# Kernel tuning notes

Measured on AMD Instinct MI355X. Metric: run time of the kernel, lower is better.

Reference implementation:

```python
import jax, jax.numpy as jnp
import numpy as np

NUM_HEADS = 12


def get_rel_pos(q_size, k_size, rel_pos):
    # relative coordinate lookup (q_size == k_size here; table has 2*size >= 2*size-1 rows)
    idx = jnp.arange(q_size)[:, None] - jnp.arange(k_size)[None, :] + (k_size - 1)
    return rel_pos[idx]  # [q_size, k_size, head_dim]


def setup_inputs() -> dict:
    key = jax.random.key(0)
    ks = jax.random.split(key, 5)
    B, H, W, E = 8, 32, 32, 768
    hd = E // NUM_HEADS
    x = jax.random.normal(ks[0], (B, H, W, E), jnp.float32)
    Wqkv = jax.random.normal(ks[1], (E, 3 * E), jnp.float32) * (E ** -0.5)
    bqkv = jnp.zeros((3 * E,), jnp.float32)
    Wproj = jax.random.normal(ks[2], (E, E), jnp.float32) * (E ** -0.5)
    bproj = jnp.zeros((E,), jnp.float32)
    rel_pos_h = jax.random.normal(ks[3], (2 * H, hd), jnp.float32) * 0.02
    rel_pos_w = jax.random.normal(ks[4], (2 * W, hd), jnp.float32) * 0.02
    return dict(x=x, Wqkv=Wqkv, bqkv=bqkv, Wproj=Wproj, bproj=bproj,
                rel_pos_h=rel_pos_h, rel_pos_w=rel_pos_w)


def reference(x, Wqkv, bqkv, Wproj, bproj, rel_pos_h, rel_pos_w):
    B, H, W, E = x.shape
    nh = NUM_HEADS
    hd = E // nh
    N = H * W
    scale = hd ** -0.5
    # QKV projection, then the exact reshape/transpose sequence of the TF module
    qkv = x.reshape(B, N, E) @ Wqkv + bqkv                       # [B, N, 3E]
    qkv = qkv.reshape(B, N, nh, hd, 3).transpose(0, 1, 2, 4, 3)  # [B, N, nh, 3, hd]
    qkv = qkv.reshape(B * nh, N, hd, 3)                          # raw row-major reshape (faithful)
    q, k, v = qkv[..., 0], qkv[..., 1], qkv[..., 2]              # each [B*nh, N, hd]
    attn = jnp.einsum('bnd,bmd->bnm', q * scale, k)              # [B*nh, N, N]
    # decomposed relative position bias (SAM-style)
    Rh = get_rel_pos(H, H, rel_pos_h)                            # [H, H, hd]
    Rw = get_rel_pos(W, W, rel_pos_w)                            # [W, W, hd]
    r_q = q.reshape(B * nh, H, W, hd)
    rel_h = jnp.einsum('bhwc,hkc->bhwk', r_q, Rh)                # [B*nh, H, W, H]
    rel_w = jnp.einsum('bhwc,wkc->bhwk', r_q, Rw)                # [B*nh, H, W, W]
    attn = (attn.reshape(B * nh, H, W, H, W)
            + rel_h[..., :, None]
            + rel_w[..., None, :]).reshape(B * nh, N, N)
    attn = jax.nn.softmax(attn, axis=-1)
    out = attn @ v                                               # [B*nh, N, hd]
    # faithful raw reshape + transpose back to [B, H, W, E]
    out = out.reshape(B, H, W, nh, hd).transpose(0, 3, 1, 2, 4).reshape(B, H, W, nh * hd)
    return out @ Wproj + bproj
```

## Files before the change

### kernel.cpp

```cpp
#include <hip/hip_runtime.h>
#include <hip/hip_bf16.h>


typedef __attribute__((ext_vector_type(8))) short short8;
typedef __attribute__((ext_vector_type(4))) float f32x4;

__global__ __launch_bounds__(256) void cast_f32_bf16(const float* __restrict__ in,
                                                     __hip_bfloat16* __restrict__ out) {
  int i = (blockIdx.x * 256 + threadIdx.x) * 4;
  float4 v = *(const float4*)&in[i];
  out[i + 0] = __float2bfloat16(v.x);
  out[i + 1] = __float2bfloat16(v.y);
  out[i + 2] = __float2bfloat16(v.z);
  out[i + 3] = __float2bfloat16(v.w);
}

__global__ __launch_bounds__(256) void transpose_cast(const float* __restrict__ in,
                                                      __hip_bfloat16* __restrict__ out,
                                                      int K, int N) {
  __shared__ float tile[32][33];
  int n0 = blockIdx.x * 32, k0 = blockIdx.y * 32;
  int tx = threadIdx.x & 31, ty = threadIdx.x >> 5;
#pragma unroll
  for (int i = 0; i < 4; ++i)
    tile[ty + i * 8][tx] = in[(size_t)(k0 + ty + i * 8) * N + n0 + tx];
  __syncthreads();
#pragma unroll
  for (int i = 0; i < 4; ++i)
    out[(size_t)(n0 + ty + i * 8) * K + k0 + tx] = __float2bfloat16(tile[tx][ty + i * 8]);
}

__device__ inline void gload16(const void* g, void* l) {
  __builtin_amdgcn_global_load_lds((const __attribute__((address_space(1))) void*)g,
                                   (__attribute__((address_space(3))) void*)l, 16, 0, 0);
}

template<int BM, bool OUT_BF16>
__global__ __launch_bounds__(256) void gemm_pipe(const __hip_bfloat16* __restrict__ A,
                                                 const __hip_bfloat16* __restrict__ Bt,
                                                 const float* __restrict__ bias,
                                                 void* __restrict__ Cout,
                                                 int N, int K) {
  constexpr int FM = BM / 32;
  constexpr int ABYTES = BM * 128;
  constexpr int AOPW = BM / 32;
  __shared__ __align__(16) char lds[2 * ABYTES + 2 * 16384];
  char* Abuf = lds;
  char* Bbuf = lds + 2 * ABYTES;
  int n0 = blockIdx.x * 128, m0 = blockIdx.y * BM;
  int tid = threadIdx.x, lane = tid & 63, wid = tid >> 6;
  int wm = wid >> 1, wn = wid & 1;
  int lr = lane & 15, lg = lane >> 4;
  int xr = lr & 7;
  int g_ = lane >> 3;
  int colsw = ((lane & 7) ^ g_) * 8;
  f32x4 acc[FM][4] = {};

#pragma unroll
  for (int j = 0; j < AOPW; ++j) {
    int op = wid * AOPW + j;
    gload16(&A[(size_t)(m0 + op * 8 + g_) * K + colsw], Abuf + op * 1024);
  }
#pragma unroll
  for (int j = 0; j < 4; ++j) {
    int op = wid * 4 + j;
    gload16(&Bt[(size_t)(n0 + op * 8 + g_) * K + colsw], Bbuf + op * 1024);
  }

  int cur = 0;
#pragma unroll 1
  for (int k0 = 0; k0 < K; k0 += 64) {
    __builtin_amdgcn_sched_barrier(0);
    __builtin_amdgcn_s_barrier();
    int kn = (k0 + 64 < K) ? k0 + 64 : k0;
#pragma unroll
    for (int j = 0; j < AOPW; ++j) {
      int op = wid * AOPW + j;
      gload16(&A[(size_t)(m0 + op * 8 + g_) * K + kn + colsw],
              Abuf + (cur ^ 1) * ABYTES + op * 1024);
    }
#pragma unroll
    for (int j = 0; j < 4; ++j) {
      int op = wid * 4 + j;
      gload16(&Bt[(size_t)(n0 + op * 8 + g_) * K + kn + colsw],
              Bbuf + (cur ^ 1) * 16384 + op * 1024);
    }
    if constexpr (BM == 128) asm volatile("s_waitcnt vmcnt(8)" ::: "memory");
    else                     asm volatile("s_waitcnt vmcnt(6)" ::: "memory");
    __builtin_amdgcn_sched_barrier(0);
    __builtin_amdgcn_s_barrier();
    __builtin_amdgcn_sched_barrier(0);

    const char* Ac = Abuf + cur * ABYTES;
    const char* Bc = Bbuf + cur * 16384;
#pragma unroll
    for (int ks = 0; ks < 2; ++ks) {
      short8 af[FM], bfr[4];
#pragma unroll
      for (int m = 0; m < FM; ++m) {
        int row = wm * (BM / 2) + m * 16 + lr;
        af[m] = *(const short8*)(Ac + row * 128 + (((ks * 4 + lg) ^ xr) * 16));
      }
#pragma unroll
      for (int n = 0; n < 4; ++n) {
        int row = wn * 64 + n * 16 + lr;
        bfr[n] = *(const short8*)(Bc + row * 128 + (((ks * 4 + lg) ^ xr) * 16));
      }
#pragma unroll
      for (int m = 0; m < FM; ++m)
#pragma unroll
        for (int n = 0; n < 4; ++n)
          acc[m][n] = __builtin_amdgcn_mfma_f32_16x16x32_bf16(af[m], bfr[n], acc[m][n], 0, 0, 0);
    }
    cur ^= 1;
  }
#pragma unroll
  for (int n = 0; n < 4; ++n) {
    int col = n0 + wn * 64 + n * 16 + lr;
    float bv = bias[col];
#pragma unroll
    for (int m = 0; m < FM; ++m) {
      int rowb = m0 + wm * (BM / 2) + m * 16 + lg * 4;
#pragma unroll
      for (int r = 0; r < 4; ++r) {
        float v = acc[m][n][r] + bv;
        if (OUT_BF16)
          ((__hip_bfloat16*)Cout)[(size_t)(rowb + r) * N + col] = __float2bfloat16(v);
        else
          ((float*)Cout)[(size_t)(rowb + r) * N + col] = v;
      }
    }
  }
}

__global__ __launch_bounds__(256) void permute_v2(const __hip_bfloat16* __restrict__ qkv,
                                                  __hip_bfloat16* __restrict__ Q,
                                                  __hip_bfloat16* __restrict__ Kd,
                                                  __hip_bfloat16* __restrict__ Vt) {
  int bh = blockIdx.y, n0 = blockIdx.x * 64;
  int tid = threadIdx.x;
  __shared__ short raw[64 * 200];
  __shared__ short vt[64][72];
  const short* src = (const short*)qkv + (size_t)(bh * 1024 + n0) * 192;
#pragma unroll
  for (int i = 0; i < 6; ++i) {
    int c16 = tid + i * 256;
    int wi = c16 / 24, off = (c16 % 24) * 8;
    *(short8*)&raw[wi * 200 + off] = *(const short8*)&src[(size_t)c16 * 8];
  }
  __syncthreads();
  int wi = tid >> 2, g4 = tid & 3;
  const short* rw_ = &raw[wi * 200];
  short8 qv[2], kv_[2];
#pragma unroll
  for (int half = 0; half < 2; ++half)
#pragma unroll
    for (int j = 0; j < 8; ++j) {
      int d2 = g4 * 16 + half * 8 + j;
      int u = 3 * d2;
      qv[half][j]  = rw_[((u) & 63) * 3 + ((u) >> 6)];
      kv_[half][j] = rw_[((u + 1) & 63) * 3 + ((u + 1) >> 6)];
      vt[d2][wi]   = rw_[((u + 2) & 63) * 3 + ((u + 2) >> 6)];
    }
  size_t base = (size_t)bh * 65536 + (size_t)(n0 + wi) * 64 + g4 * 16;
  *(short8*)&Q[base] = qv[0];
  *(short8*)&Q[base + 8] = qv[1];
  *(short8*)&Kd[base] = kv_[0];
  *(short8*)&Kd[base + 8] = kv_[1];
  __syncthreads();
  int d2r = tid >> 2;
  size_t vbase = (size_t)bh * 65536 + (size_t)d2r * 1024 + n0 + g4 * 16;
  *(short8*)&Vt[vbase]     = *(const short8*)&vt[d2r][g4 * 16];
  *(short8*)&Vt[vbase + 8] = *(const short8*)&vt[d2r][g4 * 16 + 8];
}

__device__ inline short8 cvt8(const float* p) {
  short8 r;
#pragma unroll
  for (int j = 0; j < 8; ++j) {
    __hip_bfloat16 b = __float2bfloat16(p[j]);
    r[j] = *reinterpret_cast<const short*>(&b);
  }
  return r;
}

__device__ inline unsigned packtrunc(float a, float b) {
  return __builtin_amdgcn_perm(__float_as_uint(b), __float_as_uint(a), 0x07060302u);
}

#define L2E 1.44269504088896f
__global__ __launch_bounds__(512) void attn13(const __hip_bfloat16* __restrict__ Q,
                                              const __hip_bfloat16* __restrict__ Kd,
                                              const __hip_bfloat16* __restrict__ Vt,
                                              const float* __restrict__ rph,
                                              const float* __restrict__ rpw,
                                              __hip_bfloat16* __restrict__ outp) {
  int orig = blockIdx.x;
  int xcd = orig & 7, loc = orig >> 3;
  int bh = xcd * 12 + (loc % 12);
  int qt = loc / 12;
  int tid = threadIdx.x;
  int lane = tid & 63, w = tid >> 6;
  int lr = lane & 15, lg = lane >> 4;
  int xr = lr & 7;

  __shared__ __align__(16) char lds[49152];

  const __hip_bfloat16* Qb = Q + (size_t)bh * 65536;
  const __hip_bfloat16* Kb = Kd + (size_t)bh * 65536;
  const __hip_bfloat16* Vb = Vt + (size_t)bh * 65536;

  int q0 = qt * 128 + w * 16;
  int hq = q0 >> 5;
  int wq_lane = (q0 & 31) + lr;

  short8 qf0 = *(const short8*)&Qb[(size_t)(q0 + lr) * 64 + lg * 8];
  short8 qf1 = *(const short8*)&Qb[(size_t)(q0 + lr) * 64 + 32 + lg * 8];

  char* rhb = lds + 24576 + w * 1024;
#pragma unroll
  for (int kt = 0; kt < 2; ++kt) {
    int row = hq - (kt * 16 + lr) + 31;
    const float* tp = rph + (size_t)row * 64 + lg * 8;
    short8 th0 = cvt8(tp), th1 = cvt8(tp + 32);
    f32x4 a = {};
    a = __builtin_amdgcn_mfma_f32_16x16x32_bf16(qf0, th0, a, 0, 0, 0);
    a = __builtin_amdgcn_mfma_f32_16x16x32_bf16(qf1, th1, a, 0, 0, 0);
#pragma unroll
    for (int r = 0; r < 4; ++r) {
      int q = lg * 4 + r;
      int e = kt * 16 + lr;
      int sw = ((e >> 1) ^ q) << 2;
      *(__hip_bfloat16*)(rhb + q * 64 + sw + (e & 1) * 2) = __float2bfloat16(a[r] * L2E);
    }
  }
  __hip_bfloat16* rwt = (__hip_bfloat16*)(lds + w * 2176);
#pragma unroll
  for (int jt = 0; jt < 4; ++jt) {
    const float* tp = rpw + (size_t)(jt * 16 + lr) * 64 + lg * 8;
    short8 tw0 = cvt8(tp), tw1 = cvt8(tp + 32);
    f32x4 a = {};
    a = __builtin_amdgcn_mfma_f32_16x16x32_bf16(qf0, tw0, a, 0, 0, 0);
    a = __builtin_amdgcn_mfma_f32_16x16x32_bf16(qf1, tw1, a, 0, 0, 0);
#pragma unroll
    for (int r = 0; r < 4; ++r)
      rwt[(lg * 4 + r) * 68 + jt * 16 + lr] = __float2bfloat16(a[r] * L2E);
  }
  float rwreg[8];
#pragma unroll
  for (int i = 0; i < 8; ++i) {
    int k = (i >> 2) * 16 + lg * 4 + (i & 3);
    rwreg[i] = __bfloat162float(rwt[lr * 68 + (wq_lane - k + 31)]);
  }
  __syncthreads();

  f32x4 O[4] = {};
  float m_ = -1e30f, lsum = 0.f;
  const float C = 0.125f * L2E;
  char* pc = lds + 32768 + w * 2048;
  char* vcb = lds + 16384;

  int g_ = lane >> 3;
  int colb = ((lane & 7) ^ g_) * 8;

  gload16(&Kb[(size_t)(w * 8 + g_) * 64 + colb], lds + w * 1024);

  int cur = 0;
#pragma unroll 1
  for (int kv0 = 0; kv0 < 1024; kv0 += 64) {
    __builtin_amdgcn_sched_barrier(0);
    __builtin_amdgcn_s_barrier();
    gload16(&Vb[(size_t)(w * 8 + g_) * 1024 + kv0 + colb], vcb + w * 1024);
    int nkv = (kv0 + 64 < 1024) ? kv0 + 64 : 960;
    gload16(&Kb[(size_t)(nkv + w * 8 + g_) * 64 + colb], lds + (cur ^ 1) * 8192 + w * 1024);
    asm volatile("s_waitcnt vmcnt(2)" ::: "memory");
    __builtin_amdgcn_sched_barrier(0);
    __builtin_amdgcn_s_barrier();
    __builtin_amdgcn_sched_barrier(0);

    const char* kc = lds + cur * 8192;
    short8 kf[8];
#pragma unroll
    for (int t = 0; t < 4; ++t)
#pragma unroll
      for (int h = 0; h < 2; ++h)
        kf[2 * t + h] = *(const short8*)(kc + (t * 16 + lr) * 128 + (((h * 4 + lg) ^ xr) * 16));
    f32x4 st[4];
#pragma unroll
    for (int t = 0; t < 4; ++t) {
      f32x4 z = {};
      z = __builtin_amdgcn_mfma_f32_16x16x32_bf16(kf[2 * t], qf0, z, 0, 0, 0);
      z = __builtin_amdgcn_mfma_f32_16x16x32_bf16(kf[2 * t + 1], qf1, z, 0, 0, 0);
      st[t] = z;
    }
    int s_ = kv0 >> 6;
    unsigned bu = *(const unsigned*)(rhb + lr * 64 + ((s_ ^ lr) << 2));
    float bh0 = __uint_as_float(bu << 16);
    float bh1 = __uint_as_float(bu & 0xffff0000u);
    float mx = -1e30f;
#pragma unroll
    for (int t = 0; t < 4; ++t)
#pragma unroll
      for (int r = 0; r < 4; ++r) {
        float sv = fmaf(st[t][r], C, ((t < 2) ? bh0 : bh1) + rwreg[(t & 1) * 4 + r]);
        st[t][r] = sv;
        mx = fmaxf(mx, sv);
      }
    if (!__all(mx <= m_ + 8.f)) {
      float mw = fmaxf(mx, __shfl_xor(mx, 16, 64));
      mw = fmaxf(mw, __shfl_xor(mw, 32, 64));
      float mnew = fmaxf(m_, mw);
      float al = exp2f(m_ - mnew);
      lsum *= al;
      m_ = mnew;
#pragma unroll
      for (int r = 0; r < 4; ++r) {
        float av = __shfl(al, lg * 4 + r, 64);
#pragma unroll
        for (int dt = 0; dt < 4; ++dt) O[dt][r] *= av;
      }
    }
    float sa = 0.f;
#pragma unroll
    for (int t = 0; t < 4; ++t) {
      float p0 = exp2f(st[t][0] - m_);
      float p1 = exp2f(st[t][1] - m_);
      float p2 = exp2f(st[t][2] - m_);
      float p3 = exp2f(st[t][3] - m_);
      sa += (p0 + p1) + (p2 + p3);
      uint2 wv;
      wv.x = packtrunc(p0, p1);
      wv.y = packtrunc(p2, p3);
      int slot = (2 * t + (lg >> 1)) ^ xr;
      *(uint2*)(pc + lr * 128 + slot * 16 + (lg & 1) * 8) = wv;
    }
    lsum += sa;
    short8 pf0 = *(const short8*)(pc + lr * 128 + (((0 + lg) ^ xr) * 16));
    short8 pf1 = *(const short8*)(pc + lr * 128 + (((4 + lg) ^ xr) * 16));
    asm volatile("s_waitcnt vmcnt(1)" ::: "memory");
    __builtin_amdgcn_sched_barrier(0);
    __builtin_amdgcn_s_barrier();
    __builtin_amdgcn_sched_barrier(0);
#pragma unroll
    for (int dt = 0; dt < 4; ++dt) {
      short8 vf0 = *(const short8*)(vcb + (dt * 16 + lr) * 128 + (((0 + lg) ^ xr) * 16));
      short8 vf1 = *(const short8*)(vcb + (dt * 16 + lr) * 128 + (((4 + lg) ^ xr) * 16));
      O[dt] = __builtin_amdgcn_mfma_f32_16x16x32_bf16(pf0, vf0, O[dt], 0, 0, 0);
      O[dt] = __builtin_amdgcn_mfma_f32_16x16x32_bf16(pf1, vf1, O[dt], 0, 0, 0);
    }
    cur ^= 1;
  }

  float lt = lsum;
  lt += __shfl_xor(lt, 16, 64);
  lt += __shfl_xor(lt, 32, 64);
  float linv = 1.f / lt;
#pragma unroll
  for (int r = 0; r < 4; ++r) {
    float lv = __shfl(linv, lg * 4 + r, 64);
    int n = q0 + lg * 4 + r;
#pragma unroll
    for (int dt = 0; dt < 4; ++dt) {
      int d = dt * 16 + lr;
      int Sidx = bh * 65536 + n * 64 + d;
      int b = Sidx / 786432, r1 = Sidx % 786432;
      int pp = r1 / 24576, r2 = r1 % 24576;
      int qq = r2 / 768, r3 = r2 % 768;
      int j = r3 >> 6, dd = r3 & 63;
      int P = b * 786432 + j * 65536 + pp * 2048 + qq * 64 + dd;
      outp[P] = __float2bfloat16(O[dt][r] * lv);
    }
  }
}

extern "C" void kernel_launch(void* const* d_in, const int* in_sizes, int n_in,
                              void* d_out, int out_size, void* d_ws, size_t ws_size,
                              hipStream_t stream) {
  const float* x     = (const float*)d_in[0];
  const float* Wqkv  = (const float*)d_in[1];
  const float* bqkv  = (const float*)d_in[2];
  const float* Wproj = (const float*)d_in[3];
  const float* bproj = (const float*)d_in[4];
  const float* rph   = (const float*)d_in[5];
  const float* rpw   = (const float*)d_in[6];
  float* out = (float*)d_out;
  char* ws = (char*)d_ws;

  __hip_bfloat16* xb     = (__hip_bfloat16*)(ws);
  __hip_bfloat16* wqkvT  = (__hip_bfloat16*)(ws + 12582912);
  __hip_bfloat16* wprojT = (__hip_bfloat16*)(ws + 16121856);
  __hip_bfloat16* qkvb   = (__hip_bfloat16*)(ws + 17301504);
  __hip_bfloat16* Qm     = (__hip_bfloat16*)(ws + 55050240);
  __hip_bfloat16* Km     = (__hip_bfloat16*)(ws + 67633152);
  __hip_bfloat16* Vtm    = (__hip_bfloat16*)(ws + 80216064);

  cast_f32_bf16<<<dim3(6144), dim3(256), 0, stream>>>(x, xb);
  transpose_cast<<<dim3(72, 24), dim3(256), 0, stream>>>(Wqkv, wqkvT, 768, 2304);
  transpose_cast<<<dim3(24, 24), dim3(256), 0, stream>>>(Wproj, wprojT, 768, 768);
  gemm_pipe<128, true><<<dim3(18, 64), dim3(256), 0, stream>>>(xb, wqkvT, bqkv, (void*)qkvb, 2304, 768);
  permute_v2<<<dim3(16, 96), dim3(256), 0, stream>>>(qkvb, Qm, Km, Vtm);
  attn13<<<dim3(768), dim3(512), 0, stream>>>(Qm, Km, Vtm, rph, rpw, qkvb);
  gemm_pipe<64, false><<<dim3(6, 128), dim3(256), 0, stream>>>(qkvb, wprojT, bproj, (void*)out, 768, 768);
}
```

Before: 153.2 us.

## Fuse QKV head permutation into QKV GEMM epilogue via permuted weight columns

The Wqkv transpose-cast now reorders output columns so the QKV GEMM produces Q, K and V directly in the head-split layout. The epilogue scatters bf16 results straight into Q, K and the transposed V buffers, which removes the separate permute kernel and its round trip of the qkv intermediate through memory. In exchange the epilogue stores are 2-byte scattered writes. The V-transposed writes in particular are strided by 1024 elements, so they may coalesce poorly.

```diff
diff --git a/kernel.cpp b/kernel.cpp
--- a/kernel.cpp
+++ b/kernel.cpp
@@ -30,16 +30,38 @@
     out[(size_t)(n0 + ty + i * 8) * K + k0 + tx] = __float2bfloat16(tile[tx][ty + i * 8]);
 }
 
+__global__ __launch_bounds__(256) void transpose_cast_pi(const float* __restrict__ in,
+                                                         __hip_bfloat16* __restrict__ out) {
+  __shared__ float tile[32][33];
+  int n0 = blockIdx.x * 32, k0 = blockIdx.y * 32;
+  int tx = threadIdx.x & 31, ty = threadIdx.x >> 5;
+  int j = n0 + tx;
+  int c2 = j / 768, rem = j - c2 * 768;
+  int h = rem >> 6, d2 = rem & 63;
+  int u = 3 * d2 + c2;
+  int src = h * 192 + (u & 63) * 3 + (u >> 6);
+#pragma unroll
+  for (int i = 0; i < 4; ++i)
+    tile[ty + i * 8][tx] = in[(size_t)(k0 + ty + i * 8) * 2304 + src];
+  __syncthreads();
+#pragma unroll
+  for (int i = 0; i < 4; ++i)
+    out[(size_t)(n0 + ty + i * 8) * 768 + k0 + tx] = __float2bfloat16(tile[tx][ty + i * 8]);
+}
+
 __device__ inline void gload16(const void* g, void* l) {
   __builtin_amdgcn_global_load_lds((const __attribute__((address_space(1))) void*)g,
                                    (__attribute__((address_space(3))) void*)l, 16, 0, 0);
 }
 
-template<int BM, bool OUT_BF16>
+template<int BM, int MODE>
 __global__ __launch_bounds__(256) void gemm_pipe(const __hip_bfloat16* __restrict__ A,
                                                  const __hip_bfloat16* __restrict__ Bt,
                                                  const float* __restrict__ bias,
-                                                 void* __restrict__ Cout,
+                                                 float* __restrict__ Cf32,
+                                                 __hip_bfloat16* __restrict__ Qd,
+                                                 __hip_bfloat16* __restrict__ Kdd,
+                                                 __hip_bfloat16* __restrict__ Vd,
                                                  int N, int K) {
   constexpr int FM = BM / 32;
   constexpr int ABYTES = BM * 128;
@@ -116,62 +138,38 @@
   }
 #pragma unroll
   for (int n = 0; n < 4; ++n) {
-    int col = n0 + wn * 64 + n * 16 + lr;
-    float bv = bias[col];
-#pragma unroll
-    for (int m = 0; m < FM; ++m) {
-      int rowb = m0 + wm * (BM / 2) + m * 16 + lg * 4;
-#pragma unroll
-      for (int r = 0; r < 4; ++r) {
-        float v = acc[m][n][r] + bv;
-        if (OUT_BF16)
-          ((__hip_bfloat16*)Cout)[(size_t)(rowb + r) * N + col] = __float2bfloat16(v);
-        else
-          ((float*)Cout)[(size_t)(rowb + r) * N + col] = v;
-      }
-    }
-  }
-}
-
-__global__ __launch_bounds__(256) void permute_v2(const __hip_bfloat16* __restrict__ qkv,
-                                                  __hip_bfloat16* __restrict__ Q,
-                                                  __hip_bfloat16* __restrict__ Kd,
-                                                  __hip_bfloat16* __restrict__ Vt) {
-  int bh = blockIdx.y, n0 = blockIdx.x * 64;
-  int tid = threadIdx.x;
-  __shared__ short raw[64 * 200];
-  __shared__ short vt[64][72];
-  const short* src = (const short*)qkv + (size_t)(bh * 1024 + n0) * 192;
-#pragma unroll
-  for (int i = 0; i < 6; ++i) {
-    int c16 = tid + i * 256;
-    int wi = c16 / 24, off = (c16 % 24) * 8;
-    *(short8*)&raw[wi * 200 + off] = *(const short8*)&src[(size_t)c16 * 8];
-  }
-  __syncthreads();
-  int wi = tid >> 2, g4 = tid & 3;
-  const short* rw_ = &raw[wi * 200];
-  short8 qv[2], kv_[2];
-#pragma unroll
-  for (int half = 0; half < 2; ++half)
-#pragma unroll
-    for (int j = 0; j < 8; ++j) {
-      int d2 = g4 * 16 + half * 8 + j;
-      int u = 3 * d2;
-      qv[half][j]  = rw_[((u) & 63) * 3 + ((u) >> 6)];
-      kv_[half][j] = rw_[((u + 1) & 63) * 3 + ((u + 1) >> 6)];
-      vt[d2][wi]   = rw_[((u + 2) & 63) * 3 + ((u + 2) >> 6)];
-    }
-  size_t base = (size_t)bh * 65536 + (size_t)(n0 + wi) * 64 + g4 * 16;
-  *(short8*)&Q[base] = qv[0];
-  *(short8*)&Q[base + 8] = qv[1];
-  *(short8*)&Kd[base] = kv_[0];
-  *(short8*)&Kd[base + 8] = kv_[1];
-  __syncthreads();
-  int d2r = tid >> 2;
-  size_t vbase = (size_t)bh * 65536 + (size_t)d2r * 1024 + n0 + g4 * 16;
-  *(short8*)&Vt[vbase]     = *(const short8*)&vt[d2r][g4 * 16];
-  *(short8*)&Vt[vbase + 8] = *(const short8*)&vt[d2r][g4 * 16 + 8];
+    int j = n0 + wn * 64 + n * 16 + lr;
+    if constexpr (MODE == 0) {
+      float bv = bias[j];
+#pragma unroll
+      for (int m = 0; m < FM; ++m) {
+        int rowb = m0 + wm * (BM / 2) + m * 16 + lg * 4;
+#pragma unroll
+        for (int r = 0; r < 4; ++r)
+          Cf32[(size_t)(rowb + r) * N + j] = acc[m][n][r] + bv;
+      }
+    } else {
+      int c = j / 768, rem = j - c * 768;
+      int h = rem >> 6, dd = rem & 63;
+      int u = 3 * dd + c;
+      float bv = bias[h * 192 + (u & 63) * 3 + (u >> 6)];
+      __hip_bfloat16* dst01 = (c == 0) ? Qd : Kdd;
+#pragma unroll
+      for (int m = 0; m < FM; ++m) {
+        int rowb = m0 + wm * (BM / 2) + m * 16 + lg * 4;
+#pragma unroll
+        for (int r = 0; r < 4; ++r) {
+          float v = acc[m][n][r] + bv;
+          int W = (rowb + r) * 12 + h;
+          int bh = W >> 10, n2 = W & 1023;
+          if (c < 2)
+            dst01[(size_t)bh * 65536 + n2 * 64 + dd] = __float2bfloat16(v);
+          else
+            Vd[(size_t)bh * 65536 + (size_t)dd * 1024 + n2] = __float2bfloat16(v);
+        }
+      }
+    }
+  }
 }
 
 __device__ inline short8 cvt8(const float* p) {
@@ -395,10 +393,11 @@
   __hip_bfloat16* Vtm    = (__hip_bfloat16*)(ws + 80216064);
 
   cast_f32_bf16<<<dim3(6144), dim3(256), 0, stream>>>(x, xb);
-  transpose_cast<<<dim3(72, 24), dim3(256), 0, stream>>>(Wqkv, wqkvT, 768, 2304);
+  transpose_cast_pi<<<dim3(72, 24), dim3(256), 0, stream>>>(Wqkv, wqkvT);
   transpose_cast<<<dim3(24, 24), dim3(256), 0, stream>>>(Wproj, wprojT, 768, 768);
-  gemm_pipe<128, true><<<dim3(18, 64), dim3(256), 0, stream>>>(xb, wqkvT, bqkv, (void*)qkvb, 2304, 768);
-  permute_v2<<<dim3(16, 96), dim3(256), 0, stream>>>(qkvb, Qm, Km, Vtm);
+  gemm_pipe<128, 1><<<dim3(18, 64), dim3(256), 0, stream>>>(
+      xb, wqkvT, bqkv, nullptr, Qm, Km, Vtm, 2304, 768);
   attn13<<<dim3(768), dim3(512), 0, stream>>>(Qm, Km, Vtm, rph, rpw, qkvb);
-  gemm_pipe<64, false><<<dim3(6, 128), dim3(256), 0, stream>>>(qkvb, wprojT, bproj, (void*)out, 768, 768);
-}
+  gemm_pipe<64, 0><<<dim3(6, 128), dim3(256), 0, stream>>>(
+      qkvb, wprojT, bproj, out, nullptr, nullptr, nullptr, 768, 768);
+}
```

New measurement: 171.7 us. +12.1%, slower.
